# Kernel optimization log

Measured on AMD Instinct MI355X. Metric: run time of the kernel, lower is better.

Reference implementation:

```python
import jax, jax.numpy as jnp
import numpy as np

BN_EPS = 1e-5

def _proj(x, w):
    # 1x1x1 conv, bias=False: pure channel contraction. x: [B,C,T,H,W], w: [O,C]
    return jnp.einsum('bcthw,oc->bothw', x, w)

def _maxpool222(x):
    # MaxPool3d(kernel=2, stride=2); dims are divisible by 2.
    B, C, T, H, W = x.shape
    return x.reshape(B, C, T // 2, 2, H // 2, 2, W // 2, 2).max(axis=(3, 5, 7))

def setup_inputs() -> dict:
    key = jax.random.key(0)
    ks = jax.random.split(key, 5)
    C, Ci = 256, 128
    x = jax.random.normal(ks[0], (4, C, 16, 28, 28), dtype=jnp.float32)
    sc = 1.0 / np.sqrt(C)
    theta_w = jax.random.normal(ks[1], (Ci, C), dtype=jnp.float32) * sc
    phi_w = jax.random.normal(ks[2], (Ci, C), dtype=jnp.float32) * sc
    g_w = jax.random.normal(ks[3], (Ci, C), dtype=jnp.float32) * sc
    z_w = jax.random.normal(ks[4], (C, Ci), dtype=jnp.float32) * (1.0 / np.sqrt(Ci))
    bn_gamma = jnp.ones((C,), dtype=jnp.float32)
    bn_beta = jnp.zeros((C,), dtype=jnp.float32)
    return {"x": x, "theta_w": theta_w, "phi_w": phi_w, "g_w": g_w,
            "z_w": z_w, "bn_gamma": bn_gamma, "bn_beta": bn_beta}

def reference(x, theta_w, phi_w, g_w, z_w, bn_gamma, bn_beta):
    B, C, T, H, W = x.shape
    Ci = theta_w.shape[0]
    N = T * H * W
    theta = _proj(x, theta_w).reshape(B, Ci, N)          # [B,Ci,N]
    phi = _maxpool222(_proj(x, phi_w))                   # [B,Ci,T/2,H/2,W/2]
    g = _maxpool222(_proj(x, g_w))
    Np = phi.shape[2] * phi.shape[3] * phi.shape[4]
    phi = phi.reshape(B, Ci, Np)                         # [B,Ci,Np]
    g = g.reshape(B, Ci, Np)
    attn = jnp.einsum('bcn,bcm->bnm', theta, phi)        # [B,N,Np]
    attn = jax.nn.softmax(attn, axis=-1)
    y = jnp.einsum('bnm,bcm->bcn', attn, g)              # [B,Ci,N]
    y = y.reshape(B, Ci, T, H, W)
    z = _proj(y, z_w)                                    # [B,C,T,H,W]
    # BatchNorm3d in training mode: batch stats over (B,T,H,W), biased var
    mean = z.mean(axis=(0, 2, 3, 4), keepdims=True)
    var = z.var(axis=(0, 2, 3, 4), keepdims=True)
    zn = (z - mean) * jax.lax.rsqrt(var + BN_EPS)
    zn = zn * bn_gamma[None, :, None, None, None] + bn_beta[None, :, None, None, None]
    return x + zn
```

## Files before the change

kernel.cpp:

```cpp
#include <hip/hip_runtime.h>
#include <stdint.h>

#define B_   4
#define C_   256
#define CI_  128
#define T_   16
#define H_   28
#define W_   28
#define HW_  784
#define N_   12544
#define TP_  8
#define HP_  14
#define WP_  14
#define NP_  1568
#define NP2_ 1600
#define NT_  196
#define NT2_ 98
#define NBLK_ 784
#define NBLK2_ 392
#define KVB_ 32
#define NKT_ 49

typedef __attribute__((ext_vector_type(8))) __bf16 bf16x8;
typedef __attribute__((ext_vector_type(4))) float  f32x4;

#define MFMA(a,b,c) __builtin_amdgcn_mfma_f32_16x16x32_bf16(a,b,c,0,0,0)

__device__ __forceinline__ void split_bf16(float f, __bf16& hi, __bf16& lo){
  hi = (__bf16)f;
  lo = (__bf16)(f - (float)hi);
}

__device__ __forceinline__ uint32_t pack2(float a, float b){
  union { __bf16 h; unsigned short s; } ua, ub;
  ua.h = (__bf16)a; ub.h = (__bf16)b;
  return (uint32_t)ua.s | ((uint32_t)ub.s << 16);
}

__device__ __forceinline__ void gload_lds16(const void* g, void* l){
  __builtin_amdgcn_global_load_lds((const __attribute__((address_space(1))) void*)g,
                                   (__attribute__((address_space(3))) void*)l, 16, 0, 0);
}

__global__ __launch_bounds__(256) void k_wconv(const float* __restrict__ wt, const float* __restrict__ wp,
                       const float* __restrict__ wg, const float* __restrict__ zw,
                       __bf16* __restrict__ wth, __bf16* __restrict__ wtl,
                       __bf16* __restrict__ wph, __bf16* __restrict__ wpl,
                       __bf16* __restrict__ wgh, __bf16* __restrict__ wgl,
                       __bf16* __restrict__ zwh, __bf16* __restrict__ zwl){
  int i = blockIdx.x*256 + threadIdx.x;
  if (i < 32768){
    __bf16 h, lo;
    split_bf16(wt[i], h, lo); wth[i]=h; wtl[i]=lo;
    split_bf16(wp[i], h, lo); wph[i]=h; wpl[i]=lo;
    split_bf16(wg[i], h, lo); wgh[i]=h; wgl[i]=lo;
    split_bf16(zw[i], h, lo); zwh[i]=h; zwl[i]=lo;
  }
}

__global__ __launch_bounds__(256) void k_xt(const float* __restrict__ x,
                     __bf16* __restrict__ xth, __bf16* __restrict__ xtl){
  __shared__ float tile[64][66];
  int wg = blockIdx.x;
  int nt = wg % NT_; int ct = (wg/NT_)&3; int b = wg/(NT_*4);
  int n0 = nt*64, c0 = ct*64;
  const float* xb = x + ((size_t)(b*C_ + c0))*N_ + n0;
  int tid = threadIdx.x;
  for (int it=0; it<16; ++it){
    int idx = it*256 + tid;
    int cl = idx>>6, nl = idx&63;
    tile[cl][nl] = xb[(size_t)cl*N_ + nl];
  }
  __syncthreads();
  size_t obase = ((size_t)(b*N_ + n0))*C_ + c0;
  for (int it=0; it<16; ++it){
    int idx = it*256 + tid;
    int nl = idx>>6, cl = idx&63;
    __bf16 hi, lo;
    split_bf16(tile[cl][nl], hi, lo);
    xth[obase + (size_t)nl*C_ + cl] = hi;
    xtl[obase + (size_t)nl*C_ + cl] = lo;
  }
}

__global__ __launch_bounds__(256,4) void k_proj3(const __bf16* __restrict__ xth, const __bf16* __restrict__ xtl,
                        const __bf16* __restrict__ wth, const __bf16* __restrict__ wtl,
                        const __bf16* __restrict__ wph, const __bf16* __restrict__ wpl,
                        const __bf16* __restrict__ wgh, const __bf16* __restrict__ wgl,
                        __bf16* __restrict__ th_hi, __bf16* __restrict__ th_lo,
                        float* __restrict__ phf32, __bf16* __restrict__ ggf){
  __shared__ char wbuf[2][16384];
  int wg = blockIdx.x;
  int nt = wg % NT_; int b = wg/NT_;
  int n0 = nt*64;
  int tid = threadIdx.x; int w = tid>>6; int l = tid&63; int lr = l&15; int lg = l>>4;
  int nrow = 16*w + lr;
  size_t abase = ((size_t)(b*N_ + n0 + nrow))*C_;
  bf16x8 Ah[8], Al[8];
  #pragma unroll
  for (int ks=0; ks<8; ++ks){
    Ah[ks] = *(const bf16x8*)(xth + abase + 32*ks + 8*lg);
    Al[ks] = *(const bf16x8*)(xtl + abase + 32*ks + 8*lg);
  }
  int sp_part[4]; int sp_rowc[4]; int sp_off[4];
  #pragma unroll
  for (int i=0;i<4;++i){
    int p = i*4096 + tid*16;
    sp_part[i] = p>>13;
    int row = (p>>9)&15;
    int colb = p & 511;
    sp_rowc[i] = row*C_ + ((colb ^ ((row&7)<<4)) >> 1);
    sp_off[i] = i*4096 + w*1024;
  }
  #pragma unroll
  for (int i=0;i<4;++i){
    const __bf16* src = (sp_part[i] ? wtl : wth) + sp_rowc[i];
    gload_lds16(src, &wbuf[0][sp_off[i]]);
  }
  __syncthreads();

  size_t obase = ((size_t)(b*N_ + n0))*CI_;
  int cur = 0;
  for (int pair=0; pair<24; ++pair){
    int p = pair>>3, ot = pair&7;
    if (pair < 23){
      int pn = pair+1, p2 = pn>>3, ot2 = pn&7;
      const __bf16* bh = (p2==0) ? wth : ((p2==1) ? wph : wgh);
      const __bf16* bl = (p2==0) ? wtl : ((p2==1) ? wpl : wgl);
      #pragma unroll
      for (int i=0;i<4;++i){
        const __bf16* src = (sp_part[i] ? bl : bh) + (size_t)(16*ot2)*C_ + sp_rowc[i];
        gload_lds16(src, &wbuf[cur^1][sp_off[i]]);
      }
    }
    const char* wb = wbuf[cur];
    f32x4 aHH={0.f,0.f,0.f,0.f}, aLH={0.f,0.f,0.f,0.f}, aHL={0.f,0.f,0.f,0.f};
    int swz = (lr&7)<<4;
    #pragma unroll
    for (int ks=0; ks<8; ++ks){
      int off = lr*512 + ((ks*64 + lg*16) ^ swz);
      bf16x8 Bh = *(const bf16x8*)(wb + off);
      bf16x8 Bl = *(const bf16x8*)(wb + 8192 + off);
      aHH = MFMA(Ah[ks], Bh, aHH);
      aLH = MFMA(Al[ks], Bh, aLH);
      aHL = MFMA(Ah[ks], Bl, aHL);
    }
    f32x4 acc = aHH + aLH + aHL;
    if (p == 0){
      #pragma unroll
      for (int r=0;r<4;++r){
        int n = 16*w + 4*lg + r;
        __bf16 hi, lo; split_bf16(acc[r], hi, lo);
        th_hi[obase + (size_t)n*CI_ + 16*ot + lr] = hi;
        th_lo[obase + (size_t)n*CI_ + 16*ot + lr] = lo;
      }
    } else if (p == 1){
      #pragma unroll
      for (int r=0;r<4;++r){
        int n = 16*w + 4*lg + r;
        phf32[obase + (size_t)n*CI_ + 16*ot + lr] = acc[r];
      }
    } else {
      #pragma unroll
      for (int r=0;r<4;++r){
        int n = 16*w + 4*lg + r;
        ggf[obase + (size_t)n*CI_ + 16*ot + lr] = (__bf16)acc[r];
      }
    }
    __syncthreads();
    cur ^= 1;
  }
}

__global__ __launch_bounds__(256) void k_pool(const float* __restrict__ phf32, const __bf16* __restrict__ ggf,
                       __bf16* __restrict__ phph, __bf16* __restrict__ phpl,
                       __bf16* __restrict__ ggp){
  int idx = blockIdx.x*256 + threadIdx.x;
  if (idx >= B_*NP2_*16) return;
  int c8 = idx & 15;
  int m  = (idx>>4) % NP2_;
  int b  = idx / (16*NP2_);
  if (m >= NP_){
    bf16x8 zv;
    #pragma unroll
    for (int j=0;j<8;++j) zv[j] = (__bf16)0.f;
    *(bf16x8*)(phph + ((size_t)(b*NP2_ + m))*CI_ + c8*8) = zv;
    *(bf16x8*)(phpl + ((size_t)(b*NP2_ + m))*CI_ + c8*8) = zv;
    #pragma unroll
    for (int j=0;j<8;++j) ggp[((size_t)(b*CI_ + c8*8 + j))*NP2_ + m] = (__bf16)0.f;
    return;
  }
  int tp = m/(HP_*WP_), hp = (m/WP_)%HP_, wq = m%WP_;
  int t0 = tp*2, h0 = hp*2, w0 = wq*2;
  const float*  pb = phf32 + ((size_t)b*N_)*CI_ + c8*8;
  const __bf16* gb = ggf   + ((size_t)b*N_)*CI_ + c8*8;
  float mp[8], mg[8];
  #pragma unroll
  for (int j=0;j<8;++j){ mp[j] = -3e38f; mg[j] = -3e38f; }
  #pragma unroll
  for (int dt=0; dt<2; ++dt)
  #pragma unroll
  for (int dh=0; dh<2; ++dh)
  #pragma unroll
  for (int dw=0; dw<2; ++dw){
    int n = (t0+dt)*HW_ + (h0+dh)*W_ + (w0+dw);
    f32x4 p0 = *(const f32x4*)(pb + (size_t)n*CI_);
    f32x4 p1 = *(const f32x4*)(pb + (size_t)n*CI_ + 4);
    bf16x8 vg = *(const bf16x8*)(gb + (size_t)n*CI_);
    #pragma unroll
    for (int j=0;j<4;++j){ mp[j] = fmaxf(mp[j], p0[j]); mp[4+j] = fmaxf(mp[4+j], p1[j]); }
    #pragma unroll
    for (int j=0;j<8;++j){ mg[j] = fmaxf(mg[j], (float)vg[j]); }
  }
  bf16x8 oh, ol, og;
  #pragma unroll
  for (int j=0;j<8;++j){
    __bf16 hi, lo;
    split_bf16(mp[j], hi, lo);
    oh[j] = hi; ol[j] = lo;
    og[j] = (__bf16)mg[j];
  }
  *(bf16x8*)(phph + ((size_t)(b*NP2_ + m))*CI_ + c8*8) = oh;
  *(bf16x8*)(phpl + ((size_t)(b*NP2_ + m))*CI_ + c8*8) = ol;
  #pragma unroll
  for (int j=0;j<8;++j) ggp[((size_t)(b*CI_ + c8*8 + j))*NP2_ + m] = og[j];
}

__global__ __launch_bounds__(256) void k_phmean1(const __bf16* __restrict__ phph, const __bf16* __restrict__ phpl,
                         float* __restrict__ pph){
  __shared__ float part[2][128];
  int blk = blockIdx.x;
  int b = blk >> 3, g = blk & 7;
  int tid = threadIdx.x;
  int c = tid & 127, mo = tid >> 7;
  const __bf16* ph = phph + (size_t)b*NP2_*CI_ + c;
  const __bf16* pl = phpl + (size_t)b*NP2_*CI_ + c;
  float s = 0.f;
  for (int k=0; k<98; ++k){
    int m = g + 8*(2*k + mo);
    s += (float)ph[(size_t)m*CI_] + (float)pl[(size_t)m*CI_];
  }
  part[mo][c] = s;
  __syncthreads();
  if (tid < 128) pph[(size_t)blk*128 + tid] = part[0][tid] + part[1][tid];
}

__global__ __launch_bounds__(256) void k_phmean2(const float* __restrict__ pph, float* __restrict__ phmean){
  int t = blockIdx.x*256 + threadIdx.x;
  if (t >= B_*CI_) return;
  int b = t >> 7, c = t & 127;
  float s = 0.f;
  #pragma unroll
  for (int g=0; g<8; ++g) s += pph[(size_t)(b*8+g)*128 + c];
  phmean[b*CI_ + c] = s * (1.0f/(float)NP_);
}

__global__ __launch_bounds__(256,2) void k_attn(const __bf16* __restrict__ th_hi, const __bf16* __restrict__ th_lo,
                       const __bf16* __restrict__ phph, const __bf16* __restrict__ phpl,
                       const __bf16* __restrict__ ggp, const float* __restrict__ phmean,
                       float* __restrict__ y){
  __shared__ char sbuf[2][24576];
  __shared__ float estp[128][2];
  __shared__ float est[128];
  int wg = blockIdx.x;
  int nt = wg % NT2_; int b = wg/NT2_;
  int n0 = nt*128;
  int tid = threadIdx.x; int w = tid>>6; int l = tid&63; int lr = l&15; int lg = l>>4;
  const __bf16* phb = phph + (size_t)b*NP2_*CI_;
  const __bf16* plb = phpl + (size_t)b*NP2_*CI_;
  const __bf16* ggb = ggp + (size_t)b*CI_*NP2_;

  {
    int row = tid >> 1, q = tid & 1;
    const __bf16* rh = th_hi + ((size_t)(b*N_ + n0 + row))*CI_ + 64*q;
    const __bf16* rl = th_lo + ((size_t)(b*N_ + n0 + row))*CI_ + 64*q;
    const float* pm = phmean + b*CI_ + 64*q;
    float sacc = 0.f;
    #pragma unroll
    for (int j=0;j<8;++j){
      bf16x8 vh = *(const bf16x8*)(rh + 8*j);
      bf16x8 vl = *(const bf16x8*)(rl + 8*j);
      f32x4 p0 = *(const f32x4*)(pm + 8*j);
      f32x4 p1 = *(const f32x4*)(pm + 8*j + 4);
      #pragma unroll
      for (int k=0;k<4;++k){
        sacc += ((float)vh[k]   + (float)vl[k]  )*p0[k];
        sacc += ((float)vh[4+k] + (float)vl[4+k])*p1[k];
      }
    }
    estp[row][q] = sacc;
  }
  const __bf16* sptr[6]; int sstr[6]; int soff[6];
  #pragma unroll
  for (int jj=0; jj<6; ++jj){
    int j = w*6 + jj;
    int p = j*1024 + l*16;
    int reg = p >> 13;
    int e = p & 8191;
    if (reg < 2){
      int m = e >> 8;
      int chb = (e & 255) ^ ((m & 7) << 4);
      const __bf16* base = (reg==0 ? phb : plb);
      sptr[jj] = base + (size_t)m*CI_ + (chb>>1);
      sstr[jj] = KVB_*CI_;
    } else {
      int c = e >> 6;
      int chb = (e & 63) ^ (((c >> 1) & 3) << 4);
      sptr[jj] = ggb + (size_t)c*NP2_ + (chb>>1);
      sstr[jj] = KVB_;
    }
    soff[jj] = j*1024;
  }
  __syncthreads();
  if (tid < 128) est[tid] = estp[tid][0]+estp[tid][1];

  bf16x8 Ah[2][4], Al[2][4];
  #pragma unroll
  for (int cg=0; cg<2; ++cg){
    size_t tb = ((size_t)(b*N_ + n0 + 32*w + 16*cg))*CI_ + (size_t)lr*CI_;
    #pragma unroll
    for (int ks=0; ks<4; ++ks){
      Ah[cg][ks] = *(const bf16x8*)(th_hi + tb + 32*ks + 8*lg);
      Al[cg][ks] = *(const bf16x8*)(th_lo + tb + 32*ks + 8*lg);
    }
  }
  f32x4 yacc0[8], yacc1[8];
  #pragma unroll
  for (int ct=0; ct<8; ++ct){ yacc0[ct] = (f32x4){0.f,0.f,0.f,0.f}; yacc1[ct] = (f32x4){0.f,0.f,0.f,0.f}; }
  float psum0 = 0.f, psum1 = 0.f;
  __syncthreads();
  float estl0 = est[32*w + lr];
  float estl1 = est[32*w + 16 + lr];

  #pragma unroll
  for (int jj=0; jj<6; ++jj) gload_lds16(sptr[jj], &sbuf[0][soff[jj]]);
  __syncthreads();

  int s1 = lr + (((2*lg)  )&3)*16;
  int s2 = lr + (((2*lg+1))&3)*16;
  bool hi2 = (lg >= 2);

  int cur = 0;
  for (int t=0; t<NKT_; ++t){
    if (t < NKT_-1){
      #pragma unroll
      for (int jj=0; jj<6; ++jj)
        gload_lds16(sptr[jj] + (size_t)(t+1)*sstr[jj], &sbuf[cur^1][soff[jj]]);
    }
    const char* pb_ = sbuf[cur];
    uint32_t qa00, qa01, qa10, qa11, qb00, qb01, qb10, qb11;
    #pragma unroll
    for (int mt=0; mt<2; ++mt){
      f32x4 aHH0={0.f,0.f,0.f,0.f}, aLH0={0.f,0.f,0.f,0.f}, aHL0={0.f,0.f,0.f,0.f};
      f32x4 aHH1={0.f,0.f,0.f,0.f}, aLH1={0.f,0.f,0.f,0.f}, aHL1={0.f,0.f,0.f,0.f};
      int mrow = 16*mt + lr;
      int swz = (mrow&7)<<4;
      #pragma unroll
      for (int ks=0; ks<4; ++ks){
        int off = mrow*256 + ((64*ks + 16*lg) ^ swz);
        bf16x8 Bh = *(const bf16x8*)(pb_ + off);
        bf16x8 Bl = *(const bf16x8*)(pb_ + 8192 + off);
        aHH0 = MFMA(Bh, Ah[0][ks], aHH0);
        aLH0 = MFMA(Bh, Al[0][ks], aLH0);
        aHL0 = MFMA(Bl, Ah[0][ks], aHL0);
        aHH1 = MFMA(Bh, Ah[1][ks], aHH1);
        aLH1 = MFMA(Bh, Al[1][ks], aLH1);
        aHL1 = MFMA(Bl, Ah[1][ks], aHL1);
      }
      f32x4 sv0 = aHH0 + aLH0 + aHL0;
      f32x4 sv1 = aHH1 + aLH1 + aHL1;
      float p00 = __expf(sv0[0]-estl0), p01 = __expf(sv0[1]-estl0);
      float p02 = __expf(sv0[2]-estl0), p03 = __expf(sv0[3]-estl0);
      float p10 = __expf(sv1[0]-estl1), p11 = __expf(sv1[1]-estl1);
      float p12 = __expf(sv1[2]-estl1), p13 = __expf(sv1[3]-estl1);
      psum0 += (p00 + p01) + (p02 + p03);
      psum1 += (p10 + p11) + (p12 + p13);
      uint32_t da0 = pack2(p00,p01), da1 = pack2(p02,p03);
      uint32_t db0 = pack2(p10,p11), db1 = pack2(p12,p13);
      if (mt == 0){ qa00 = da0; qa01 = da1; qb00 = db0; qb01 = db1; }
      else        { qa10 = da0; qa11 = da1; qb10 = db0; qb11 = db1; }
    }
    uint32_t ba00 = __shfl(qa00, s1, 64), ba10 = __shfl(qa10, s1, 64);
    uint32_t ba01 = __shfl(qa01, s1, 64), ba11 = __shfl(qa11, s1, 64);
    uint32_t ca00 = __shfl(qa00, s2, 64), ca10 = __shfl(qa10, s2, 64);
    uint32_t ca01 = __shfl(qa01, s2, 64), ca11 = __shfl(qa11, s2, 64);
    union { uint32_t u[4]; bf16x8 v; } pa0;
    pa0.u[0] = hi2 ? ba10 : ba00;
    pa0.u[1] = hi2 ? ba11 : ba01;
    pa0.u[2] = hi2 ? ca10 : ca00;
    pa0.u[3] = hi2 ? ca11 : ca01;
    uint32_t bb00 = __shfl(qb00, s1, 64), bb10 = __shfl(qb10, s1, 64);
    uint32_t bb01 = __shfl(qb01, s1, 64), bb11 = __shfl(qb11, s1, 64);
    uint32_t cb00 = __shfl(qb00, s2, 64), cb10 = __shfl(qb10, s2, 64);
    uint32_t cb01 = __shfl(qb01, s2, 64), cb11 = __shfl(qb11, s2, 64);
    union { uint32_t u[4]; bf16x8 v; } pa1;
    pa1.u[0] = hi2 ? bb10 : bb00;
    pa1.u[1] = hi2 ? bb11 : bb01;
    pa1.u[2] = hi2 ? cb10 : cb00;
    pa1.u[3] = hi2 ? cb11 : cb01;
    #pragma unroll
    for (int ct=0; ct<8; ++ct){
      int c = 16*ct + lr;
      int goff = 16384 + c*64 + ((16*lg) ^ (((c>>1)&3)<<4));
      bf16x8 Gf = *(const bf16x8*)(pb_ + goff);
      yacc0[ct] = MFMA(pa0.v, Gf, yacc0[ct]);
      yacc1[ct] = MFMA(pa1.v, Gf, yacc1[ct]);
    }
    __syncthreads();
    cur ^= 1;
  }
  float rs0 = psum0;
  rs0 += __shfl_xor(rs0, 16, 64); rs0 += __shfl_xor(rs0, 32, 64);
  float rs1 = psum1;
  rs1 += __shfl_xor(rs1, 16, 64); rs1 += __shfl_xor(rs1, 32, 64);
  float inv0 = 1.0f / rs0, inv1 = 1.0f / rs1;
  float ivr0[4], ivr1[4];
  #pragma unroll
  for (int r=0; r<4; ++r){
    ivr0[r] = __shfl(inv0, 4*lg + r, 64);
    ivr1[r] = __shfl(inv1, 4*lg + r, 64);
  }
  float* yb0 = y + ((size_t)(b*N_ + n0 + 32*w))*CI_;
  float* yb1 = y + ((size_t)(b*N_ + n0 + 32*w + 16))*CI_;
  #pragma unroll
  for (int ct=0; ct<8; ++ct){
    #pragma unroll
    for (int r=0;r<4;++r){
      yb0[(size_t)(4*lg+r)*CI_ + 16*ct + lr] = yacc0[ct][r] * ivr0[r];
      yb1[(size_t)(4*lg+r)*CI_ + 16*ct + lr] = yacc1[ct][r] * ivr1[r];
    }
  }
}

__global__ __launch_bounds__(256,3) void k_zproj(const float* __restrict__ y,
                        const __bf16* __restrict__ zwh, const __bf16* __restrict__ zwl,
                        __bf16* __restrict__ z, float* __restrict__ pS, float* __restrict__ pQ){
  __shared__ float zt[64][68];
  __shared__ float red[4][256][2];
  __shared__ char wbuf[2][8192];
  int wg = blockIdx.x; int nt = wg % NT_; int b = wg/NT_; int n0 = nt*64;
  int tid = threadIdx.x; int w = tid>>6; int l = tid&63; int lr = l&15; int lg = l>>4;
  const float* yb = y + ((size_t)(b*N_ + n0 + 16*w))*CI_ + (size_t)lr*CI_;
  bf16x8 Ah[4], Al[4];
  #pragma unroll
  for (int ks=0;ks<4;++ks){
    f32x4 a0 = *(const f32x4*)(yb + 32*ks + 8*lg);
    f32x4 a1 = *(const f32x4*)(yb + 32*ks + 8*lg + 4);
    #pragma unroll
    for (int j=0;j<4;++j){
      __bf16 h0,l0,h1,l1;
      split_bf16(a0[j], h0, l0);
      split_bf16(a1[j], h1, l1);
      Ah[ks][j]   = h0; Al[ks][j]   = l0;
      Ah[ks][4+j] = h1; Al[ks][4+j] = l1;
    }
  }
  int sp_part[2]; int sp_rowc[2]; int sp_off[2];
  #pragma unroll
  for (int i=0;i<2;++i){
    int p = i*4096 + tid*16;
    sp_part[i] = p>>12;
    int row = (p>>8)&15;
    int colb = p & 255;
    sp_rowc[i] = row*CI_ + ((colb ^ ((row&7)<<4)) >> 1);
    sp_off[i] = i*4096 + w*1024;
  }
  #pragma unroll
  for (int i=0;i<2;++i){
    const __bf16* src = (sp_part[i] ? zwl : zwh) + sp_rowc[i];
    gload_lds16(src, &wbuf[0][sp_off[i]]);
  }
  __syncthreads();

  __bf16* zb = z + (size_t)b*C_*N_ + n0;
  int cur = 0;
  for (int og=0; og<4; ++og){
    #pragma unroll
    for (int oi=0; oi<4; ++oi){
      int ot = og*4 + oi;
      if (ot < 15){
        #pragma unroll
        for (int i=0;i<2;++i){
          const __bf16* src = (sp_part[i] ? zwl : zwh) + (size_t)(16*(ot+1))*CI_ + sp_rowc[i];
          gload_lds16(src, &wbuf[cur^1][sp_off[i]]);
        }
      }
      const char* wb = wbuf[cur];
      f32x4 aHH = {0.f,0.f,0.f,0.f}, aLH = {0.f,0.f,0.f,0.f}, aHL = {0.f,0.f,0.f,0.f};
      int swz = (lr&7)<<4;
      #pragma unroll
      for (int ks=0;ks<4;++ks){
        int off = lr*256 + ((ks*64 + lg*16) ^ swz);
        bf16x8 Bh = *(const bf16x8*)(wb + off);
        bf16x8 Bl = *(const bf16x8*)(wb + 4096 + off);
        aHH = MFMA(Ah[ks], Bh, aHH);
        aLH = MFMA(Al[ks], Bh, aLH);
        aHL = MFMA(Ah[ks], Bl, aHL);
      }
      f32x4 acc = aHH + aLH + aHL;
      float s1=0.f, s2=0.f;
      #pragma unroll
      for (int r=0;r<4;++r){
        float v = acc[r];
        int nl = 16*w + 4*lg + r;
        zt[16*oi+lr][nl] = v;
        s1 += v; s2 += v*v;
      }
      s1 += __shfl_xor(s1,16,64); s1 += __shfl_xor(s1,32,64);
      s2 += __shfl_xor(s2,16,64); s2 += __shfl_xor(s2,32,64);
      if (lg==0){ red[w][16*ot+lr][0] = s1; red[w][16*ot+lr][1] = s2; }
      if (oi < 3){ __syncthreads(); cur ^= 1; }
    }
    __syncthreads();
    #pragma unroll
    for (int it=0; it<2; ++it){
      int idx = it*256 + tid;
      int ol = idx>>3, cc = idx&7;
      f32x4 v0 = *(const f32x4*)(&zt[ol][cc*8]);
      f32x4 v1 = *(const f32x4*)(&zt[ol][cc*8+4]);
      bf16x8 o8;
      #pragma unroll
      for (int j=0;j<4;++j){ o8[j] = (__bf16)v0[j]; o8[4+j] = (__bf16)v1[j]; }
      *(bf16x8*)(zb + (size_t)(og*64 + ol)*N_ + cc*8) = o8;
    }
    __syncthreads();
    cur ^= 1;
  }
  float t1 = red[0][tid][0]+red[1][tid][0]+red[2][tid][0]+red[3][tid][0];
  float t2 = red[0][tid][1]+red[1][tid][1]+red[2][tid][1]+red[3][tid][1];
  pS[(size_t)wg*256 + tid] = t1;
  pQ[(size_t)wg*256 + tid] = t2;
}

__global__ __launch_bounds__(256) void k_stats(const float* __restrict__ pS, const float* __restrict__ pQ,
                        const float* __restrict__ gamma, const float* __restrict__ beta,
                        float* __restrict__ coef){
  int o = blockIdx.x; int t = threadIdx.x;
  float s=0.f, q=0.f;
  for (int i=t; i<NBLK_; i+=256){ s += pS[(size_t)i*256+o]; q += pQ[(size_t)i*256+o]; }
  __shared__ float rs[4], rq[4];
  #pragma unroll
  for (int sh=32; sh; sh>>=1){ s += __shfl_down(s,sh,64); q += __shfl_down(q,sh,64); }
  int w = t>>6;
  if ((t&63)==0){ rs[w]=s; rq[w]=q; }
  __syncthreads();
  if (t==0){
    s = rs[0]+rs[1]+rs[2]+rs[3]; q = rq[0]+rq[1]+rq[2]+rq[3];
    float inv = 1.0f/(float)(B_*N_);
    float mean = s*inv, var = q*inv - mean*mean;
    float a = gamma[o]*rsqrtf(var + 1e-5f);
    coef[o] = a; coef[256+o] = beta[o] - mean*a;
  }
}

__global__ __launch_bounds__(256) void k_final(const float* __restrict__ x, const __bf16* __restrict__ z,
                        const float* __restrict__ coef, float* __restrict__ out){
  uint32_t i = blockIdx.x*256 + threadIdx.x;
  uint32_t e0 = i*8u;
  if (e0 >= (uint32_t)(B_*C_*N_)) return;
  int o = (int)((e0 / (uint32_t)N_) % (uint32_t)C_);
  float a = coef[o], b2 = coef[256+o];
  bf16x8 zv = *(const bf16x8*)(z + e0);
  f32x4 x0 = *(const f32x4*)(x + e0);
  f32x4 x1 = *(const f32x4*)(x + e0 + 4);
  f32x4 r0, r1;
  #pragma unroll
  for (int j=0;j<4;++j){
    r0[j] = x0[j] + (float)zv[j]*a + b2;
    r1[j] = x1[j] + (float)zv[4+j]*a + b2;
  }
  *(f32x4*)(out + e0) = r0;
  *(f32x4*)(out + e0 + 4) = r1;
}

extern "C" void kernel_launch(void* const* d_in, const int* in_sizes, int n_in,
                              void* d_out, int out_size, void* d_ws, size_t ws_size,
                              hipStream_t stream){
  const float* x     = (const float*)d_in[0];
  const float* wt    = (const float*)d_in[1];
  const float* wp    = (const float*)d_in[2];
  const float* wg    = (const float*)d_in[3];
  const float* zw    = (const float*)d_in[4];
  const float* gamma = (const float*)d_in[5];
  const float* beta  = (const float*)d_in[6];
  float* out = (float*)d_out;
  char* ws = (char*)d_ws;
  size_t off = 0;
  auto alloc = [&](size_t bytes)->void*{ void* p = ws + off; off = (off + bytes + 255) & ~(size_t)255; return p; };
  __bf16* xth  = (__bf16*)alloc((size_t)B_*N_*C_*2);
  __bf16* xtl  = (__bf16*)alloc((size_t)B_*N_*C_*2);
  float*  phf32= (float*)alloc((size_t)B_*N_*CI_*4);
  __bf16* ggf  = (__bf16*)alloc((size_t)B_*N_*CI_*2);
  __bf16* th_hi= (__bf16*)alloc((size_t)B_*N_*CI_*2);
  __bf16* th_lo= (__bf16*)alloc((size_t)B_*N_*CI_*2);
  __bf16* wth  = (__bf16*)alloc(32768*2);
  __bf16* wtl  = (__bf16*)alloc(32768*2);
  __bf16* wph  = (__bf16*)alloc(32768*2);
  __bf16* wpl  = (__bf16*)alloc(32768*2);
  __bf16* wgh  = (__bf16*)alloc(32768*2);
  __bf16* wgl  = (__bf16*)alloc(32768*2);
  __bf16* zwh  = (__bf16*)alloc(32768*2);
  __bf16* zwl  = (__bf16*)alloc(32768*2);
  __bf16* phph = (__bf16*)alloc((size_t)B_*NP2_*CI_*2);
  __bf16* phpl = (__bf16*)alloc((size_t)B_*NP2_*CI_*2);
  __bf16* ggp  = (__bf16*)alloc((size_t)B_*CI_*NP2_*2);
  float*  pS   = (float*)alloc((size_t)NBLK_*256*4);
  float*  pQ   = (float*)alloc((size_t)NBLK_*256*4);
  float*  coef = (float*)alloc(512*4);
  float*  phmean = (float*)alloc(B_*CI_*4);
  float*  pph  = (float*)alloc((size_t)B_*8*128*4);
  float* y = (float*)xth;
  __bf16* z = (__bf16*)phf32;

  k_wconv<<<128, 256, 0, stream>>>(wt, wp, wg, zw, wth, wtl, wph, wpl, wgh, wgl, zwh, zwl);
  k_xt<<<B_*4*NT_, 256, 0, stream>>>(x, xth, xtl);
  k_proj3<<<NBLK_, 256, 0, stream>>>(xth, xtl, wth, wtl, wph, wpl, wgh, wgl, th_hi, th_lo, phf32, ggf);
  k_pool<<<(B_*NP2_*16 + 255)/256, 256, 0, stream>>>(phf32, ggf, phph, phpl, ggp);
  k_phmean1<<<B_*8, 256, 0, stream>>>(phph, phpl, pph);
  k_phmean2<<<2, 256, 0, stream>>>(pph, phmean);
  k_attn<<<NBLK2_, 256, 0, stream>>>(th_hi, th_lo, phph, phpl, ggp, phmean, y);
  k_zproj<<<NBLK_, 256, 0, stream>>>(y, zwh, zwl, z, pS, pQ);
  k_stats<<<256, 256, 0, stream>>>(pS, pQ, gamma, beta, coef);
  k_final<<<(B_*C_*N_/8 + 255)/256, 256, 0, stream>>>(x, z, coef, out);
}
```

Measured before the change: 242.7 us.

## Fuse x transpose and bf16 split into projection kernel loads

Removes the separate transpose kernel that wrote hi/lo bf16 copies of x in channel-last layout. The projection kernel now reads x directly from its original layout with channel-strided loads and splits it into hi/lo bf16 in registers. This avoids a full write and reread of the transposed copy and one kernel launch. The trade-off is less coalesced global loads, with 64-byte segments per lane group, inside the projection kernel.

```diff
diff --git a/kernel.cpp b/kernel.cpp
--- a/kernel.cpp
+++ b/kernel.cpp
@@ -58,32 +58,7 @@
   }
 }
 
-__global__ __launch_bounds__(256) void k_xt(const float* __restrict__ x,
-                     __bf16* __restrict__ xth, __bf16* __restrict__ xtl){
-  __shared__ float tile[64][66];
-  int wg = blockIdx.x;
-  int nt = wg % NT_; int ct = (wg/NT_)&3; int b = wg/(NT_*4);
-  int n0 = nt*64, c0 = ct*64;
-  const float* xb = x + ((size_t)(b*C_ + c0))*N_ + n0;
-  int tid = threadIdx.x;
-  for (int it=0; it<16; ++it){
-    int idx = it*256 + tid;
-    int cl = idx>>6, nl = idx&63;
-    tile[cl][nl] = xb[(size_t)cl*N_ + nl];
-  }
-  __syncthreads();
-  size_t obase = ((size_t)(b*N_ + n0))*C_ + c0;
-  for (int it=0; it<16; ++it){
-    int idx = it*256 + tid;
-    int nl = idx>>6, cl = idx&63;
-    __bf16 hi, lo;
-    split_bf16(tile[cl][nl], hi, lo);
-    xth[obase + (size_t)nl*C_ + cl] = hi;
-    xtl[obase + (size_t)nl*C_ + cl] = lo;
-  }
-}
-
-__global__ __launch_bounds__(256,4) void k_proj3(const __bf16* __restrict__ xth, const __bf16* __restrict__ xtl,
+__global__ __launch_bounds__(256,4) void k_proj3(const float* __restrict__ x,
                         const __bf16* __restrict__ wth, const __bf16* __restrict__ wtl,
                         const __bf16* __restrict__ wph, const __bf16* __restrict__ wpl,
                         const __bf16* __restrict__ wgh, const __bf16* __restrict__ wgl,
@@ -95,12 +70,16 @@
   int n0 = nt*64;
   int tid = threadIdx.x; int w = tid>>6; int l = tid&63; int lr = l&15; int lg = l>>4;
   int nrow = 16*w + lr;
-  size_t abase = ((size_t)(b*N_ + n0 + nrow))*C_;
+  const float* xb = x + (size_t)b*C_*N_ + (n0 + nrow);
   bf16x8 Ah[8], Al[8];
   #pragma unroll
   for (int ks=0; ks<8; ++ks){
-    Ah[ks] = *(const bf16x8*)(xth + abase + 32*ks + 8*lg);
-    Al[ks] = *(const bf16x8*)(xtl + abase + 32*ks + 8*lg);
+    #pragma unroll
+    for (int j=0;j<8;++j){
+      float v = xb[(size_t)(32*ks + 8*lg + j)*N_];
+      __bf16 hi, lo; split_bf16(v, hi, lo);
+      Ah[ks][j] = hi; Al[ks][j] = lo;
+    }
   }
   int sp_part[4]; int sp_rowc[4]; int sp_off[4];
   #pragma unroll
@@ -587,8 +566,7 @@
   char* ws = (char*)d_ws;
   size_t off = 0;
   auto alloc = [&](size_t bytes)->void*{ void* p = ws + off; off = (off + bytes + 255) & ~(size_t)255; return p; };
-  __bf16* xth  = (__bf16*)alloc((size_t)B_*N_*C_*2);
-  __bf16* xtl  = (__bf16*)alloc((size_t)B_*N_*C_*2);
+  float*  y    = (float*)alloc((size_t)B_*N_*CI_*4);
   float*  phf32= (float*)alloc((size_t)B_*N_*CI_*4);
   __bf16* ggf  = (__bf16*)alloc((size_t)B_*N_*CI_*2);
   __bf16* th_hi= (__bf16*)alloc((size_t)B_*N_*CI_*2);
@@ -609,12 +587,10 @@
   float*  coef = (float*)alloc(512*4);
   float*  phmean = (float*)alloc(B_*CI_*4);
   float*  pph  = (float*)alloc((size_t)B_*8*128*4);
-  float* y = (float*)xth;
   __bf16* z = (__bf16*)phf32;
 
   k_wconv<<<128, 256, 0, stream>>>(wt, wp, wg, zw, wth, wtl, wph, wpl, wgh, wgl, zwh, zwl);
-  k_xt<<<B_*4*NT_, 256, 0, stream>>>(x, xth, xtl);
-  k_proj3<<<NBLK_, 256, 0, stream>>>(xth, xtl, wth, wtl, wph, wpl, wgh, wgl, th_hi, th_lo, phf32, ggf);
+  k_proj3<<<NBLK_, 256, 0, stream>>>(x, wth, wtl, wph, wpl, wgh, wgl, th_hi, th_lo, phf32, ggf);
   k_pool<<<(B_*NP2_*16 + 255)/256, 256, 0, stream>>>(phf32, ggf, phph, phpl, ggp);
   k_phmean1<<<B_*8, 256, 0, stream>>>(phph, phpl, pph);
   k_phmean2<<<2, 256, 0, stream>>>(pph, phmean);
```

Measured after the change: 226.5 us. 6.7% less time.
